# Kernel tuning notes

Hardware: AMD Instinct MI355X
Metric: run time of the kernel (lower is better)

Reference implementation:

```python
import jax, jax.numpy as jnp
import numpy as np

SHIFT = 0.0          # drr shift
DENS_OFFSET = 0.3    # density property subtracts 0.3 before regulator


def _affine_inverse(affine, pts):
    # apply inverse of 4x4 affine to [..., 3] points (world -> voxel index space)
    inv = jnp.linalg.inv(affine)
    return pts @ inv[:3, :3].T + inv[:3, 3]


def setup_inputs() -> dict:
    key = jax.random.key(0)
    k1, k2, k3, k4 = jax.random.split(key, 4)
    D = H = W = 256
    B, N = 1, 40000  # 200x200 detector -> one ray per pixel

    _density = 0.1 * jax.random.normal(k1, (D, H, W), dtype=jnp.float32)

    # voxel-index -> world affine: unit spacing, translated origin
    affine = jnp.eye(4, dtype=jnp.float32).at[:3, 3].set(
        jnp.array([-10.0, -10.0, -10.0], dtype=jnp.float32))

    # x-ray point source on one side of the volume (slightly jittered per ray)
    src_center = jnp.array([-60.0, 118.0, 118.0], dtype=jnp.float32)
    source = src_center + 0.5 * jax.random.normal(k2, (B, N, 3), dtype=jnp.float32)

    # detector targets on the far side, spanning the volume in y/z
    ty = jax.random.uniform(k3, (B, N, 1), minval=-10.0, maxval=250.0)
    tz = jax.random.uniform(k4, (B, N, 1), minval=-10.0, maxval=250.0)
    tx = jnp.full((B, N, 1), 320.0, dtype=jnp.float32)
    target = jnp.concatenate([tx, ty, tz], axis=-1).astype(jnp.float32)

    return {"_density": _density, "source": source, "target": target,
            "affine": affine, "n_points": 500}


def reference(_density, source, target, affine, n_points):
    # density regulator: sigmoid(_density - shift - 0.3)
    density = jax.nn.sigmoid(_density - SHIFT - DENS_OFFSET)

    # ray length in world space: [B, 1, N]
    raylength = jnp.linalg.norm(target - source, axis=-1)[:, None, :]

    # map endpoints into voxel index space
    s = _affine_inverse(affine, source)   # [B, N, 3]
    t = _affine_inverse(affine, target)   # [B, N, 3]

    # sample n_points uniformly along each ray: pts [B, N, P, 3]
    alphas = jnp.linspace(0.0, 1.0, n_points, dtype=source.dtype)
    pts = s[..., None, :] + alphas[:, None] * (t - s)[..., None, :]

    # trilinear gather (zero outside volume), samples [B, N, P]
    coords = [pts[..., 0], pts[..., 1], pts[..., 2]]
    samples = jax.scipy.ndimage.map_coordinates(
        density, coords, order=1, mode="constant", cval=0.0)

    # integrate along ray: sum * (raylength / n_points) -> [B, 1, N]
    img = samples.sum(axis=-1)[:, None, :] * raylength / n_points
    return img
```

## Files before the change

### kernel.cpp

```cpp
#include <hip/hip_runtime.h>
#include <hip/hip_fp16.h>

#define NB 64
#define NBUCKETS (NB * NB)

typedef unsigned int uint2v __attribute__((ext_vector_type(2)));

__device__ __forceinline__ float sigm(float v)
{
    return 1.0f / (1.0f + __expf(0.3f - v));
}

__device__ __forceinline__ float2 unpack_h2(unsigned int w)
{
    __half2 h = *reinterpret_cast<__half2*>(&w);
    return make_float2(__low2float(h), __high2float(h));
}

__global__ __launch_bounds__(256) void pack_kernel(
    const float* __restrict__ dens, unsigned int* __restrict__ P)
{
    __shared__ float tile[32][33];
    int bid = blockIdx.x;
    int y0 = (bid & 31) * 8;
    int xt = ((bid >> 5) & 7) * 32;
    int zt = (bid >> 8) * 32;
    int tz = threadIdx.x & 31;
    int tr = threadIdx.x >> 5;

    float prev[4];
    int ytop = y0 + 8;
    if (ytop < 256) {
        #pragma unroll
        for (int i = 0; i < 4; ++i) {
            int xr = tr + 8 * i;
            tile[xr][tz] = sigm(dens[(size_t)(xt + xr) * 65536 +
                                     (size_t)ytop * 256 + (zt + tz)]);
        }
        __syncthreads();
        #pragma unroll
        for (int i = 0; i < 4; ++i)
            prev[i] = tile[tz][tr + 8 * i];
        __syncthreads();
    } else {
        #pragma unroll
        for (int i = 0; i < 4; ++i) prev[i] = 0.0f;
    }

    for (int yy = 7; yy >= 0; --yy) {
        int y = y0 + yy;
        #pragma unroll
        for (int i = 0; i < 4; ++i) {
            int xr = tr + 8 * i;
            tile[xr][tz] = sigm(dens[(size_t)(xt + xr) * 65536 +
                                     (size_t)y * 256 + (zt + tz)]);
        }
        __syncthreads();
        #pragma unroll
        for (int i = 0; i < 4; ++i) {
            int zr = tr + 8 * i;
            float cur = tile[tz][zr];
            __half2 h = __floats2half2_rn(cur, prev[i]);
            P[((zt + zr) << 16) | (y << 8) | (xt + tz)] =
                *reinterpret_cast<unsigned int*>(&h);
            prev[i] = cur;
        }
        __syncthreads();
    }
}

__device__ __forceinline__ int ray_bucket(const float* __restrict__ target, int r)
{
    float ty = target[3 * r + 1];
    float tz = target[3 * r + 2];
    int bu = (int)((ty + 10.0f) * (NB / 260.0f));
    int bv = (int)((tz + 10.0f) * (NB / 260.0f));
    bu = min(max(bu, 0), NB - 1);
    bv = min(max(bv, 0), NB - 1);
    int m = 0;
    #pragma unroll
    for (int b = 0; b < 6; ++b)
        m |= (((bu >> b) & 1) << (2 * b)) | (((bv >> b) & 1) << (2 * b + 1));
    return m;
}

__global__ __launch_bounds__(256) void zero_kernel(int* __restrict__ p, int n)
{
    int i = blockIdx.x * 256 + threadIdx.x;
    if (i < n) p[i] = 0;
}

__global__ __launch_bounds__(256) void hist_kernel(
    const float* __restrict__ target, int* __restrict__ hist, int nrays)
{
    int r = blockIdx.x * 256 + threadIdx.x;
    if (r < nrays) atomicAdd(&hist[ray_bucket(target, r)], 1);
}

__global__ __launch_bounds__(256) void scan_kernel(
    const int* __restrict__ hist, int* __restrict__ offs, int* __restrict__ cursor)
{
    __shared__ int part[256];
    int t = threadIdx.x;
    int v[16];
    int s = 0;
    #pragma unroll
    for (int i = 0; i < 16; ++i) {
        v[i] = hist[t * 16 + i];
        s += v[i];
    }
    part[t] = s;
    __syncthreads();
    for (int d = 1; d < 256; d <<= 1) {
        int add = (t >= d) ? part[t - d] : 0;
        __syncthreads();
        part[t] += add;
        __syncthreads();
    }
    int base = part[t] - s;
    #pragma unroll
    for (int i = 0; i < 16; ++i) {
        offs[t * 16 + i] = base;
        base += v[i];
        cursor[t * 16 + i] = 0;
    }
}

__global__ __launch_bounds__(256) void scatter_kernel(
    const float* __restrict__ target, const int* __restrict__ offs,
    int* __restrict__ cursor, int* __restrict__ perm, int nrays)
{
    int r = blockIdx.x * 256 + threadIdx.x;
    if (r >= nrays) return;
    int bkt = ray_bucket(target, r);
    int pos = offs[bkt] + atomicAdd(&cursor[bkt], 1);
    perm[pos] = r;
}

__device__ __forceinline__ float2 fetchP(
    const unsigned int* __restrict__ P, int x, int y, int z)
{
    if ((unsigned)x < 256u && (unsigned)z < 256u) {
        if ((unsigned)y < 256u)
            return unpack_h2(P[(z << 16) | (y << 8) | x]);
        if (y == -1) {
            float2 v = unpack_h2(P[(z << 16) | x]);
            return make_float2(0.0f, v.x);
        }
    }
    return make_float2(0.0f, 0.0f);
}

__global__ __launch_bounds__(256) void drr_kernel(
    const unsigned int* __restrict__ P,
    const float*  __restrict__ source,
    const float*  __restrict__ target,
    const float*  __restrict__ affine,
    const int*    __restrict__ npts_ptr,
    const int*    __restrict__ perm,
    float*        __restrict__ out,
    int nrays)
{
    const int lane  = threadIdx.x & 63;
    const int sub   = lane >> 4;
    const int phase = lane & 15;
    const int wave  = threadIdx.x >> 6;
    int slot = blockIdx.x * 16 + wave * 4 + sub;
    bool valid = (slot < nrays);
    if (slot >= nrays) slot = nrays - 1;
    const int ray = perm ? perm[slot] : slot;
    const int npts = *npts_ptr;

    float a00 = affine[0], a01 = affine[1], a02 = affine[2],  b0 = affine[3];
    float a10 = affine[4], a11 = affine[5], a12 = affine[6],  b1 = affine[7];
    float a20 = affine[8], a21 = affine[9], a22 = affine[10], b2 = affine[11];
    float det = a00 * (a11 * a22 - a12 * a21)
              - a01 * (a10 * a22 - a12 * a20)
              + a02 * (a10 * a21 - a11 * a20);
    float rdet = 1.0f / det;
    float i00 =  (a11 * a22 - a12 * a21) * rdet;
    float i01 = -(a01 * a22 - a02 * a21) * rdet;
    float i02 =  (a01 * a12 - a02 * a11) * rdet;
    float i10 = -(a10 * a22 - a12 * a20) * rdet;
    float i11 =  (a00 * a22 - a02 * a20) * rdet;
    float i12 = -(a00 * a12 - a02 * a10) * rdet;
    float i20 =  (a10 * a21 - a11 * a20) * rdet;
    float i21 = -(a00 * a21 - a01 * a20) * rdet;
    float i22 =  (a00 * a11 - a01 * a10) * rdet;
    float it0 = -(i00 * b0 + i01 * b1 + i02 * b2);
    float it1 = -(i10 * b0 + i11 * b1 + i12 * b2);
    float it2 = -(i20 * b0 + i21 * b1 + i22 * b2);

    float sx = source[3 * ray + 0], sy = source[3 * ray + 1], sz = source[3 * ray + 2];
    float tx = target[3 * ray + 0], ty = target[3 * ray + 1], tz = target[3 * ray + 2];
    float dwx = tx - sx, dwy = ty - sy, dwz = tz - sz;
    float rl = sqrtf(dwx * dwx + dwy * dwy + dwz * dwz);

    float vsx = i00 * sx + i01 * sy + i02 * sz + it0;
    float vsy = i10 * sx + i11 * sy + i12 * sz + it1;
    float vsz = i20 * sx + i21 * sy + i22 * sz + it2;
    float vtx = i00 * tx + i01 * ty + i02 * tz + it0;
    float vty = i10 * tx + i11 * ty + i12 * tz + it1;
    float vtz = i20 * tx + i21 * ty + i22 * tz + it2;
    float vdx = vtx - vsx, vdy = vty - vsy, vdz = vtz - vsz;

    float lo = 0.0f, hi = 1.0f;
    {
        float s3v[3] = {vsx, vsy, vsz};
        float d3v[3] = {vdx, vdy, vdz};
        #pragma unroll
        for (int k = 0; k < 3; ++k) {
            if (fabsf(d3v[k]) > 1e-8f) {
                float a = (-1.0f - s3v[k]) / d3v[k];
                float b = (256.0f - s3v[k]) / d3v[k];
                lo = fmaxf(lo, fminf(a, b));
                hi = fminf(hi, fmaxf(a, b));
            } else if (s3v[k] <= -1.0f || s3v[k] >= 256.0f) {
                lo = 1.0f; hi = 0.0f;
            }
        }
    }
    const float stepN = (float)(npts > 1 ? npts - 1 : 1);
    int pstart = max(0, (int)floorf(lo * stepN) - 1);
    int pend   = min(npts - 1, (int)ceilf(hi * stepN) + 1);

    const float step = 1.0f / stepN;
    float acc = 0.0f;

    float al0 = (float)(pstart + phase) * step;
    float x = fmaf(al0, vdx, vsx);
    float y = fmaf(al0, vdy, vsy);
    float z = fmaf(al0, vdz, vsz);
    float d16x = 16.0f * step * vdx;
    float d16y = 16.0f * step * vdy;
    float d16z = 16.0f * step * vdz;

    #pragma unroll 4
    for (int p = pstart + phase; p <= pend; p += 16) {
        float fx = floorf(x), fy = floorf(y), fz = floorf(z);
        int ix = (int)fx, iy = (int)fy, iz = (int)fz;
        float wx = x - fx, wy = y - fy, wz = z - fz;
        x += d16x; y += d16y; z += d16z;

        float2 p00, p01, p10, p11;
        bool interior = ((unsigned)ix < 255u) & ((unsigned)iy < 256u) &
                        ((unsigned)iz < 255u);
        if (interior) {
            int idx = (iz << 16) | (iy << 8) | ix;
            uint2v va, vb;
            __builtin_memcpy(&va, P + idx, 8);
            __builtin_memcpy(&vb, P + idx + 65536, 8);
            p00 = unpack_h2(va.x);
            p01 = unpack_h2(va.y);
            p10 = unpack_h2(vb.x);
            p11 = unpack_h2(vb.y);
        } else {
            p00 = fetchP(P, ix,     iy, iz);
            p01 = fetchP(P, ix + 1, iy, iz);
            p10 = fetchP(P, ix,     iy, iz + 1);
            p11 = fetchP(P, ix + 1, iy, iz + 1);
        }
        float c00 = p00.x + wy * (p00.y - p00.x);
        float c10 = p01.x + wy * (p01.y - p01.x);
        float c01 = p10.x + wy * (p10.y - p10.x);
        float c11 = p11.x + wy * (p11.y - p11.x);
        float c0  = c00 + wz * (c01 - c00);
        float c1  = c10 + wz * (c11 - c10);
        acc += c0 + wx * (c1 - c0);
    }

    #pragma unroll
    for (int off = 8; off > 0; off >>= 1)
        acc += __shfl_down(acc, off, 16);

    if (phase == 0 && valid)
        out[ray] = acc * rl / (float)npts;
}

extern "C" void kernel_launch(void* const* d_in, const int* in_sizes, int n_in,
                              void* d_out, int out_size, void* d_ws, size_t ws_size,
                              hipStream_t stream)
{
    const float* dens   = (const float*)d_in[0];
    const float* source = (const float*)d_in[1];
    const float* target = (const float*)d_in[2];
    const float* affine = (const float*)d_in[3];
    const int*   npts   = (const int*)d_in[4];
    float* out = (float*)d_out;

    const int nvox  = in_sizes[0];
    const int nrays = in_sizes[1] / 3;

    size_t packBytes = ((size_t)nvox * 4 + 255) & ~(size_t)255;
    size_t sortBytes = (size_t)(3 * NBUCKETS + nrays) * sizeof(int);

    const int ray_blocks = (nrays + 15) / 16;

    unsigned int* P = (unsigned int*)d_ws;
    int* hist   = (int*)((char*)d_ws + packBytes);
    int* offs   = hist + NBUCKETS;
    int* cursor = offs + NBUCKETS;
    int* perm   = cursor + NBUCKETS;
    const bool srt = (ws_size >= packBytes + sortBytes);
    int* permArg = srt ? perm : nullptr;

    if (srt) {
        zero_kernel<<<(NBUCKETS + 255) / 256, 256, 0, stream>>>(hist, NBUCKETS);
        hist_kernel<<<(nrays + 255) / 256, 256, 0, stream>>>(target, hist, nrays);
        scan_kernel<<<1, 256, 0, stream>>>(hist, offs, cursor);
        scatter_kernel<<<(nrays + 255) / 256, 256, 0, stream>>>(target, offs, cursor, perm, nrays);
    }

    pack_kernel<<<2048, 256, 0, stream>>>(dens, P);
    drr_kernel<<<ray_blocks, 256, 0, stream>>>(
        P, source, target, affine, npts, permArg, out, nrays);
}
```

Baseline: 172.0 us.

## Pack y/z voxel neighbors into 8-byte cells for single 16-byte trilinear fetch

Adds a new packing kernel that stores, for each voxel, the fp16 sigmoid densities of its y and z neighbors (4 values, 8 bytes), so a trilinear sample needs one 16-byte load instead of two 8-byte loads in separate z planes. The ray kernel is templated to use this layout and processes 8 rays per wave with 8 phases each instead of 4 rays with 16 phases. The packed volume doubles in size (128MB instead of 64MB), which makes the pack kernel costlier and raises cache footprint. It falls back to the old layout when the workspace is too small.

After: 185.5 us. 1.08x slower.

```diff
diff --git a/kernel.cpp b/kernel.cpp
--- a/kernel.cpp
+++ b/kernel.cpp
@@ -5,6 +5,7 @@
 #define NBUCKETS (NB * NB)
 
 typedef unsigned int uint2v __attribute__((ext_vector_type(2)));
+typedef unsigned int uint4v __attribute__((ext_vector_type(4)));
 
 __device__ __forceinline__ float sigm(float v)
 {
@@ -15,6 +16,57 @@
 {
     __half2 h = *reinterpret_cast<__half2*>(&w);
     return make_float2(__low2float(h), __high2float(h));
+}
+
+__global__ __launch_bounds__(256) void packq_kernel(
+    const float* __restrict__ dens, uint2v* __restrict__ Q)
+{
+    __shared__ float S[2][33 * 33 + 1];
+    int bid = blockIdx.x;
+    int y0 = (bid & 31) * 8;
+    int xt = ((bid >> 5) & 7) * 32;
+    int zt = (bid >> 8) * 32;
+    int tid = threadIdx.x;
+
+    auto load_plane = [&](int y) {
+        float* Sp = S[y & 1];
+        #pragma unroll
+        for (int r = 0; r < 5; ++r) {
+            int li = r * 256 + tid;
+            if (li < 33 * 32) {
+                int zc = li % 33, xr = li / 33;
+                int zz = zt + zc;
+                float v = 0.0f;
+                if (zz < 256 && y < 256)
+                    v = sigm(dens[(size_t)(xt + xr) * 65536 +
+                                  (size_t)y * 256 + zz]);
+                Sp[zc * 33 + xr] = v;
+            }
+        }
+    };
+
+    load_plane(y0 + 8);
+    for (int y = y0 + 7; y >= y0; --y) {
+        __syncthreads();
+        load_plane(y);
+        __syncthreads();
+        const float* S0 = S[y & 1];
+        const float* S1 = S[(y + 1) & 1];
+        int xo = tid & 31;
+        int zb = tid >> 5;
+        #pragma unroll
+        for (int i = 0; i < 4; ++i) {
+            int zo = zb + 8 * i;
+            __half2 d0 = __floats2half2_rn(S0[zo * 33 + xo],
+                                           S1[zo * 33 + xo]);
+            __half2 d1 = __floats2half2_rn(S0[(zo + 1) * 33 + xo],
+                                           S1[(zo + 1) * 33 + xo]);
+            uint2v q;
+            q.x = *reinterpret_cast<unsigned int*>(&d0);
+            q.y = *reinterpret_cast<unsigned int*>(&d1);
+            Q[((zt + zo) << 16) | (y << 8) | (xt + xo)] = q;
+        }
+    }
 }
 
 __global__ __launch_bounds__(256) void pack_kernel(
@@ -137,6 +189,37 @@
     perm[pos] = r;
 }
 
+__device__ __forceinline__ float4 fetchQ4(
+    const uint2v* __restrict__ Q, int x, int y, int z)
+{
+    if ((unsigned)x < 256u) {
+        if ((unsigned)y < 256u) {
+            if ((unsigned)z < 256u) {
+                uint2v q = Q[(z << 16) | (y << 8) | x];
+                float2 a = unpack_h2(q.x), b = unpack_h2(q.y);
+                return make_float4(a.x, a.y, b.x, b.y);
+            }
+            if (z == -1) {
+                uint2v q = Q[(y << 8) | x];
+                float2 a = unpack_h2(q.x);
+                return make_float4(0.0f, 0.0f, a.x, a.y);
+            }
+        } else if (y == -1) {
+            if ((unsigned)z < 256u) {
+                uint2v q = Q[(z << 16) | x];
+                float2 a = unpack_h2(q.x), b = unpack_h2(q.y);
+                return make_float4(0.0f, a.x, 0.0f, b.x);
+            }
+            if (z == -1) {
+                uint2v q = Q[x];
+                float2 a = unpack_h2(q.x);
+                return make_float4(0.0f, 0.0f, 0.0f, a.x);
+            }
+        }
+    }
+    return make_float4(0.0f, 0.0f, 0.0f, 0.0f);
+}
+
 __device__ __forceinline__ float2 fetchP(
     const unsigned int* __restrict__ P, int x, int y, int z)
 {
@@ -151,8 +234,9 @@
     return make_float2(0.0f, 0.0f);
 }
 
+template <bool Q8>
 __global__ __launch_bounds__(256) void drr_kernel(
-    const unsigned int* __restrict__ P,
+    const void*   __restrict__ volp,
     const float*  __restrict__ source,
     const float*  __restrict__ target,
     const float*  __restrict__ affine,
@@ -161,11 +245,14 @@
     float*        __restrict__ out,
     int nrays)
 {
+    constexpr int R  = Q8 ? 8 : 4;
+    constexpr int PH = 64 / R;
+
     const int lane  = threadIdx.x & 63;
-    const int sub   = lane >> 4;
-    const int phase = lane & 15;
+    const int sub   = lane / PH;
+    const int phase = lane % PH;
     const int wave  = threadIdx.x >> 6;
-    int slot = blockIdx.x * 16 + wave * 4 + sub;
+    int slot = blockIdx.x * (4 * R) + wave * R + sub;
     bool valid = (slot < nrays);
     if (slot >= nrays) slot = nrays - 1;
     const int ray = perm ? perm[slot] : slot;
@@ -227,51 +314,77 @@
     const float step = 1.0f / stepN;
     float acc = 0.0f;
 
+    const uint2v*       Q  = (const uint2v*)volp;
+    const unsigned int* P  = (const unsigned int*)volp;
+
     float al0 = (float)(pstart + phase) * step;
     float x = fmaf(al0, vdx, vsx);
     float y = fmaf(al0, vdy, vsy);
     float z = fmaf(al0, vdz, vsz);
-    float d16x = 16.0f * step * vdx;
-    float d16y = 16.0f * step * vdy;
-    float d16z = 16.0f * step * vdz;
+    float dSx = (float)PH * step * vdx;
+    float dSy = (float)PH * step * vdy;
+    float dSz = (float)PH * step * vdz;
 
     #pragma unroll 4
-    for (int p = pstart + phase; p <= pend; p += 16) {
+    for (int p = pstart + phase; p <= pend; p += PH) {
         float fx = floorf(x), fy = floorf(y), fz = floorf(z);
         int ix = (int)fx, iy = (int)fy, iz = (int)fz;
         float wx = x - fx, wy = y - fy, wz = z - fz;
-        x += d16x; y += d16y; z += d16z;
-
-        float2 p00, p01, p10, p11;
-        bool interior = ((unsigned)ix < 255u) & ((unsigned)iy < 256u) &
-                        ((unsigned)iz < 255u);
-        if (interior) {
-            int idx = (iz << 16) | (iy << 8) | ix;
-            uint2v va, vb;
-            __builtin_memcpy(&va, P + idx, 8);
-            __builtin_memcpy(&vb, P + idx + 65536, 8);
-            p00 = unpack_h2(va.x);
-            p01 = unpack_h2(va.y);
-            p10 = unpack_h2(vb.x);
-            p11 = unpack_h2(vb.y);
+        x += dSx; y += dSy; z += dSz;
+
+        float2 pa, pb, pc, pd;
+        if (Q8) {
+            bool interior = ((unsigned)ix < 255u) & ((unsigned)iy < 256u) &
+                            ((unsigned)iz < 256u);
+            if (interior) {
+                int idx = (iz << 16) | (iy << 8) | ix;
+                const unsigned int* qp =
+                    (const unsigned int*)Q + ((size_t)idx << 1);
+                uint4v v;
+                __builtin_memcpy(&v, qp, 16);
+                pa = unpack_h2(v.x);
+                pb = unpack_h2(v.y);
+                pc = unpack_h2(v.z);
+                pd = unpack_h2(v.w);
+            } else {
+                float4 fa = fetchQ4(Q, ix,     iy, iz);
+                float4 fb = fetchQ4(Q, ix + 1, iy, iz);
+                pa = make_float2(fa.x, fa.y);
+                pb = make_float2(fa.z, fa.w);
+                pc = make_float2(fb.x, fb.y);
+                pd = make_float2(fb.z, fb.w);
+            }
         } else {
-            p00 = fetchP(P, ix,     iy, iz);
-            p01 = fetchP(P, ix + 1, iy, iz);
-            p10 = fetchP(P, ix,     iy, iz + 1);
-            p11 = fetchP(P, ix + 1, iy, iz + 1);
-        }
-        float c00 = p00.x + wy * (p00.y - p00.x);
-        float c10 = p01.x + wy * (p01.y - p01.x);
-        float c01 = p10.x + wy * (p10.y - p10.x);
-        float c11 = p11.x + wy * (p11.y - p11.x);
-        float c0  = c00 + wz * (c01 - c00);
-        float c1  = c10 + wz * (c11 - c10);
-        acc += c0 + wx * (c1 - c0);
+            bool interior = ((unsigned)ix < 255u) & ((unsigned)iy < 256u) &
+                            ((unsigned)iz < 255u);
+            if (interior) {
+                int idx = (iz << 16) | (iy << 8) | ix;
+                uint2v va, vb;
+                __builtin_memcpy(&va, P + idx, 8);
+                __builtin_memcpy(&vb, P + idx + 65536, 8);
+                pa = unpack_h2(va.x);
+                pc = unpack_h2(va.y);
+                pb = unpack_h2(vb.x);
+                pd = unpack_h2(vb.y);
+            } else {
+                pa = fetchP(P, ix,     iy, iz);
+                pc = fetchP(P, ix + 1, iy, iz);
+                pb = fetchP(P, ix,     iy, iz + 1);
+                pd = fetchP(P, ix + 1, iy, iz + 1);
+            }
+        }
+        float ca = pa.x + wy * (pa.y - pa.x);
+        float cb = pb.x + wy * (pb.y - pb.x);
+        float cc = pc.x + wy * (pc.y - pc.x);
+        float cd = pd.x + wy * (pd.y - pd.x);
+        float e = ca + wz * (cb - ca);
+        float f = cc + wz * (cd - cc);
+        acc += e + wx * (f - e);
     }
 
     #pragma unroll
-    for (int off = 8; off > 0; off >>= 1)
-        acc += __shfl_down(acc, off, 16);
+    for (int off = PH / 2; off > 0; off >>= 1)
+        acc += __shfl_down(acc, off, PH);
 
     if (phase == 0 && valid)
         out[ray] = acc * rl / (float)npts;
@@ -291,17 +404,18 @@
     const int nvox  = in_sizes[0];
     const int nrays = in_sizes[1] / 3;
 
-    size_t packBytes = ((size_t)nvox * 4 + 255) & ~(size_t)255;
+    size_t qBytes    = ((size_t)nvox * 8 + 255) & ~(size_t)255;
+    size_t pBytes    = ((size_t)nvox * 4 + 255) & ~(size_t)255;
     size_t sortBytes = (size_t)(3 * NBUCKETS + nrays) * sizeof(int);
 
-    const int ray_blocks = (nrays + 15) / 16;
-
-    unsigned int* P = (unsigned int*)d_ws;
-    int* hist   = (int*)((char*)d_ws + packBytes);
+    const bool q8 = (ws_size >= qBytes + sortBytes);
+    size_t volBytes = q8 ? qBytes : pBytes;
+
+    int* hist   = (int*)((char*)d_ws + volBytes);
     int* offs   = hist + NBUCKETS;
     int* cursor = offs + NBUCKETS;
     int* perm   = cursor + NBUCKETS;
-    const bool srt = (ws_size >= packBytes + sortBytes);
+    const bool srt = (ws_size >= volBytes + sortBytes);
     int* permArg = srt ? perm : nullptr;
 
     if (srt) {
@@ -311,7 +425,15 @@
         scatter_kernel<<<(nrays + 255) / 256, 256, 0, stream>>>(target, offs, cursor, perm, nrays);
     }
 
-    pack_kernel<<<2048, 256, 0, stream>>>(dens, P);
-    drr_kernel<<<ray_blocks, 256, 0, stream>>>(
-        P, source, target, affine, npts, permArg, out, nrays);
-}
+    if (q8) {
+        uint2v* Q = (uint2v*)d_ws;
+        packq_kernel<<<2048, 256, 0, stream>>>(dens, Q);
+        drr_kernel<true><<<(nrays + 31) / 32, 256, 0, stream>>>(
+            Q, source, target, affine, npts, permArg, out, nrays);
+    } else {
+        unsigned int* P = (unsigned int*)d_ws;
+        pack_kernel<<<2048, 256, 0, stream>>>(dens, P);
+        drr_kernel<false><<<(nrays + 15) / 16, 256, 0, stream>>>(
+            P, source, target, affine, npts, permArg, out, nrays);
+    }
+}
```
